# Kernel optimization log

Hardware: AMD Instinct MI355X
Metric: run time of the kernel (lower is better)

The kernel has to match this reference:

```python
import jax, jax.numpy as jnp
import numpy as np

N = 100000      # nodes
E = 1600000     # edges
D_IN = 256
D_HID = 256
D_OUT = 256
DROP_P = 0.5


def setup_inputs() -> dict:
    key = jax.random.key(0)
    ks = jax.random.split(key, 10)
    s = 1.0 / np.sqrt(D_HID)
    return {
        "z": jax.random.normal(ks[0], (N, D_OUT), jnp.float32),
        "omega": jax.random.normal(ks[1], (N, D_IN), jnp.float32),
        "edge_index": jax.random.randint(ks[2], (2, E), 0, N, jnp.int32),
        "W_lin": jax.random.normal(ks[3], (D_IN, D_HID), jnp.float32) * s,
        "b_lin": jnp.zeros((D_HID,), jnp.float32),
        "W_g1": jax.random.normal(ks[4], (D_HID, D_HID), jnp.float32) * s,
        "b_g1": jnp.zeros((D_HID,), jnp.float32),
        "W_g2": jax.random.normal(ks[5], (D_HID, D_OUT), jnp.float32) * s,
        "b_g2": jnp.zeros((D_OUT,), jnp.float32),
        "mask1": jax.random.bernoulli(ks[6], 1.0 - DROP_P, (N, D_HID)),
        "mask2": jax.random.bernoulli(ks[7], 1.0 - DROP_P, (N, D_HID)),
    }


def _gcn_norm(edge_index):
    # add self-loops, symmetric normalization deg^-1/2 * deg^-1/2
    loop = jnp.arange(N, dtype=edge_index.dtype)
    src = jnp.concatenate([edge_index[0], loop])
    dst = jnp.concatenate([edge_index[1], loop])
    deg = jax.ops.segment_sum(jnp.ones_like(dst, jnp.float32), dst, num_segments=N)
    dinv = jax.lax.rsqrt(deg)  # deg >= 1 because of self-loops
    norm = dinv[src] * dinv[dst]  # [E+N]
    return src, dst, norm


def _gcn_conv(x, W, b, src, dst, norm):
    h = x @ W                                  # [N, d_out]
    msg = h[src] * norm[:, None]               # gather over edges
    out = jax.ops.segment_sum(msg, dst, num_segments=N)  # scatter-add
    return out + b


def _dropout(x, mask):
    return jnp.where(mask, x * (1.0 / (1.0 - DROP_P)), 0.0)


def reference(z, omega, edge_index, W_lin, b_lin, W_g1, b_g1, W_g2, b_g2, mask1, mask2):
    src, dst, norm = _gcn_norm(edge_index)
    # layer 0: Linear + relu + dropout
    h = _dropout(jax.nn.relu(omega @ W_lin + b_lin), mask1)
    # layer 1: GCNConv + relu + dropout
    h = _dropout(jax.nn.relu(_gcn_conv(h, W_g1, b_g1, src, dst, norm)), mask2)
    # layer 2: GCNConv
    h = _gcn_conv(h, W_g2, b_g2, src, dst, norm)
    return z * h
```

## Files before the change

kernel.cpp:

```cpp
#include <hip/hip_runtime.h>
#include <stdint.h>

#define NN 100000
#define EE 1600000
#define DD 256
#define GB0 1563
#define NFILL 1024
#define NSUB 128

typedef __bf16 bf16;
typedef __attribute__((ext_vector_type(8))) __bf16 bf16x8;
typedef __attribute__((ext_vector_type(4))) float f32x4;
typedef __attribute__((ext_vector_type(4))) unsigned int u32x4;
typedef __attribute__((ext_vector_type(8))) unsigned short u16x8;

typedef __attribute__((address_space(1))) const unsigned int g_u32c;
typedef __attribute__((address_space(3))) unsigned int lds_u32;

__device__ __forceinline__ float bflo(unsigned int u) {
    union { unsigned int u; float f; } x; x.u = u << 16; return x.f;
}
__device__ __forceinline__ float bfhi(unsigned int u) {
    union { unsigned int u; float f; } x; x.u = u & 0xFFFF0000u; return x.f;
}
__device__ __forceinline__ unsigned short f2bf(float f) {
    return __builtin_bit_cast(unsigned short, (__bf16)f);
}

__global__ __launch_bounds__(256) void fillprep_k(
    const int* __restrict__ src, const int* __restrict__ dst,
    int* __restrict__ cnt, int* __restrict__ cs,
    const float* __restrict__ W0, const float* __restrict__ W1,
    const float* __restrict__ W2, bf16* __restrict__ T0,
    bf16* __restrict__ T1, bf16* __restrict__ T2,
    const unsigned int* __restrict__ m, int* __restrict__ flag) {
    int b = blockIdx.x;
    if (b < NFILL) {
        int prt = b & 7;
        int sub = b >> 3;
        int lo = prt * (NN >> 3);
        int hi = (prt == 7) ? NN : lo + (NN >> 3);
        const int per = EE / NSUB;
        int e0 = sub * per;
        int e1 = (sub == NSUB - 1) ? EE : e0 + per;
        for (int e = e0 + threadIdx.x; e < e1; e += 256) {
            int d = dst[e];
            if (d >= lo && d < hi) {
                int s = src[e];
                int slot = atomicAdd(&cnt[d], 1);
                if (slot < 64) cs[(d << 6) + slot] = s;
            }
        }
        return;
    }
    b -= NFILL;
    if (b == 192) {
        if (threadIdx.x < 64) {
            unsigned int v = m[threadIdx.x];
            int bad = (v > 1u && v != 0x3F800000u) ? 1 : 0;
            unsigned long long bl = __ballot(bad);
            if (threadIdx.x == 0) *flag = (bl != 0ull) ? 1 : 0;
        }
        return;
    }
    const float* W = b < 64 ? W0 : (b < 128 ? W1 : W2);
    bf16*       T  = b < 64 ? T0 : (b < 128 ? T1 : T2);
    int bb = b & 63;
    __shared__ float tile[32][33];
    int bx = bb & 7, by = bb >> 3;
    int tx = threadIdx.x & 31, ty = threadIdx.x >> 5;
    #pragma unroll
    for (int r = 0; r < 32; r += 8)
        tile[ty + r][tx] = W[(size_t)(by * 32 + ty + r) * DD + bx * 32 + tx];
    __syncthreads();
    #pragma unroll
    for (int r = 0; r < 32; r += 8)
        T[(size_t)(bx * 32 + ty + r) * DD + by * 32 + tx] = (bf16)tile[tx][ty + r];
}

template <int EPI, int F32A>
__device__ __forceinline__ void gemm_body(
    const void* __restrict__ Ap, const bf16* __restrict__ Wt,
    const float* __restrict__ bias, const void* __restrict__ mask,
    const int* __restrict__ flagp, const float* __restrict__ z,
    void* __restrict__ outp, bf16* As, bf16* Bs, int m0) {
    int tid = threadIdx.x;
    int wid = tid >> 6, lane = tid & 63;
    int lr = lane & 15, lk = lane >> 4;
    int rx = lr & 7;

    f32x4 acc[4][4] = {};

    for (int k0 = 0; k0 < DD; k0 += 64) {
        #pragma unroll
        for (int i = 0; i < 2; i++) {
            int f = i * 256 + tid;
            int row = f >> 3;
            int cl  = f & 7;
            int cg  = cl ^ (row & 7);
            int gr = m0 + row; if (gr > NN - 1) gr = NN - 1;
            if (F32A) {
                const float* sp = (const float*)Ap + (size_t)gr * DD + k0 + cl * 8;
                float4 v0 = *(const float4*)sp;
                float4 v1 = *(const float4*)(sp + 4);
                u16x8 o = { f2bf(v0.x), f2bf(v0.y), f2bf(v0.z), f2bf(v0.w),
                            f2bf(v1.x), f2bf(v1.y), f2bf(v1.z), f2bf(v1.w) };
                *(u16x8*)(As + row * 64 + cg * 8) = o;
            } else {
                __builtin_amdgcn_global_load_lds(
                    (g_u32c*)((const bf16*)Ap + (size_t)gr * DD + k0 + cg * 8),
                    (lds_u32*)(As + (size_t)f * 8), 16, 0, 0);
            }
        }
        #pragma unroll
        for (int i = 0; i < 8; i++) {
            int f = i * 256 + tid;
            int row = f >> 3;
            int cg  = (f & 7) ^ (row & 7);
            __builtin_amdgcn_global_load_lds(
                (g_u32c*)(Wt + (size_t)row * DD + k0 + cg * 8),
                (lds_u32*)(Bs + (size_t)f * 8), 16, 0, 0);
        }
        __syncthreads();
        #pragma unroll
        for (int kk = 0; kk < 2; kk++) {
            bf16x8 af[4], bfr[4];
            #pragma unroll
            for (int mi = 0; mi < 4; mi++)
                af[mi] = *(const bf16x8*)(As + (mi * 16 + lr) * 64 + (((kk * 4 + lk) ^ rx) * 8));
            #pragma unroll
            for (int ni = 0; ni < 4; ni++)
                bfr[ni] = *(const bf16x8*)(Bs + (wid * 64 + ni * 16 + lr) * 64 + (((kk * 4 + lk) ^ rx) * 8));
            #pragma unroll
            for (int mi = 0; mi < 4; mi++)
                #pragma unroll
                for (int ni = 0; ni < 4; ni++)
                    acc[mi][ni] = __builtin_amdgcn_mfma_f32_16x16x32_bf16(
                        bfr[ni], af[mi], acc[mi][ni], 0, 0, 0);
        }
        __syncthreads();
    }

    int bm = (EPI == 1) ? *flagp : 0;
    #pragma unroll
    for (int mi = 0; mi < 4; mi++) {
        int gr = m0 + mi * 16 + lr;
        if (gr >= NN) continue;
        #pragma unroll
        for (int ni = 0; ni < 4; ni++) {
            int gc = wid * 64 + ni * 16 + lk * 4;
            size_t idx = (size_t)gr * DD + gc;
            float4 b4 = *(const float4*)(bias + gc);
            float v0 = acc[mi][ni][0] + b4.x;
            float v1 = acc[mi][ni][1] + b4.y;
            float v2 = acc[mi][ni][2] + b4.z;
            float v3 = acc[mi][ni][3] + b4.w;
            if (EPI == 1) {
                v0 = fmaxf(v0, 0.f); v1 = fmaxf(v1, 0.f);
                v2 = fmaxf(v2, 0.f); v3 = fmaxf(v3, 0.f);
                if (bm) {
                    uchar4 u = *(const uchar4*)((const unsigned char*)mask + idx);
                    v0 *= u.x ? 2.f : 0.f; v1 *= u.y ? 2.f : 0.f;
                    v2 *= u.z ? 2.f : 0.f; v3 *= u.w ? 2.f : 0.f;
                } else {
                    uint4 u = *(const uint4*)((const unsigned int*)mask + idx);
                    v0 *= u.x ? 2.f : 0.f; v1 *= u.y ? 2.f : 0.f;
                    v2 *= u.z ? 2.f : 0.f; v3 *= u.w ? 2.f : 0.f;
                }
                ushort4 o = { f2bf(v0), f2bf(v1), f2bf(v2), f2bf(v3) };
                *(ushort4*)((unsigned short*)outp + idx) = o;
            } else {
                f32x4 zz = __builtin_nontemporal_load((const f32x4*)(z + idx));
                f32x4 o = { v0 * zz.x, v1 * zz.y, v2 * zz.z, v3 * zz.w };
                __builtin_nontemporal_store(o, (f32x4*)((float*)outp + idx));
            }
        }
    }
}

__global__ __launch_bounds__(256) void gemm0_k(
    const float* __restrict__ omega, const bf16* __restrict__ Wt,
    const float* __restrict__ bias, const void* __restrict__ mask,
    const int* __restrict__ flagp, bf16* __restrict__ outp) {
    __shared__ __align__(16) bf16 As[64 * 64];
    __shared__ __align__(16) bf16 Bs[256 * 64];
    int m0 = blockIdx.x * 64;
    if (m0 >= NN) return;
    gemm_body<1, 1>(omega, Wt, bias, mask, flagp, nullptr, outp, As, Bs, m0);
}

template <int ID, int EPI>
__global__ __launch_bounds__(256) void gemm_k(
    const bf16* __restrict__ Ap, const bf16* __restrict__ Wt,
    const float* __restrict__ bias, const void* __restrict__ mask,
    const int* __restrict__ flagp, const float* __restrict__ z,
    void* __restrict__ outp) {
    __shared__ __align__(16) bf16 As[64 * 64];
    __shared__ __align__(16) bf16 Bs[256 * 64];
    int m0 = blockIdx.x * 64;
    if (m0 >= NN) return;
    gemm_body<EPI, 0>(Ap, Wt, bias, mask, flagp, z, outp, As, Bs, m0);
}

#define AGG_GET(J, UVAR, MVAR)                                                   \
    {                                                                            \
        int _i = 2 * (J) + half;                                                 \
        int _s = __shfl(sl, _i & 63);                                            \
        float _w = __shfl(wl, _i & 63);                                          \
        MVAR = (_i < nume) ? _w : 0.f;                                           \
        UVAR = *(const u32x4*)(tb + (((size_t)(unsigned)_s) << 9) + lcoff);      \
    }
#define AGG_FMA(UVAR, MVAR)                                                      \
    {                                                                            \
        acc[0] = fmaf(MVAR, bflo(UVAR.x), acc[0]);                               \
        acc[1] = fmaf(MVAR, bfhi(UVAR.x), acc[1]);                               \
        acc[2] = fmaf(MVAR, bflo(UVAR.y), acc[2]);                               \
        acc[3] = fmaf(MVAR, bfhi(UVAR.y), acc[3]);                               \
        acc[4] = fmaf(MVAR, bflo(UVAR.z), acc[4]);                               \
        acc[5] = fmaf(MVAR, bfhi(UVAR.z), acc[5]);                               \
        acc[6] = fmaf(MVAR, bflo(UVAR.w), acc[6]);                               \
        acc[7] = fmaf(MVAR, bfhi(UVAR.w), acc[7]);                               \
    }

__global__ __launch_bounds__(256) void agg_k(
    const bf16* __restrict__ t, const int* __restrict__ cnt,
    const int* __restrict__ cs, bf16* __restrict__ out) {
    int node = blockIdx.x * 4 + (threadIdx.x >> 6);
    if (node >= NN) return;
    int lane = threadIdx.x & 63;
    int half = lane >> 5;
    int lc = lane & 31;
    int cn = cnt[node];
    int nume = cn > 63 ? 63 : cn;

    float acc[8] = {};
    const char* tb = (const char*)t;
    size_t lcoff = (size_t)(lc << 4);

    if (nume > 0) {
        int base = node << 6;
        int sl = 0; float wl = 0.f;
        if (lane < nume) {
            sl = __builtin_nontemporal_load(cs + base + lane);
            wl = rsqrtf((float)(cnt[sl] + 1));
        }
        int nit = (nume + 1) >> 1;

        u32x4 ua, ub, uc, ud;
        float ma, mb, mc, md;
        AGG_GET(0, ua, ma);
        AGG_GET(1, ub, mb);
        AGG_GET(2, uc, mc);
        int j = 0;
        for (; j + 3 < nit; j += 4) {
            AGG_GET(j + 3, ud, md); AGG_FMA(ua, ma);
            AGG_GET(j + 4, ua, ma); AGG_FMA(ub, mb);
            AGG_GET(j + 5, ub, mb); AGG_FMA(uc, mc);
            AGG_GET(j + 6, uc, mc); AGG_FMA(ud, md);
        }
        int rem = nit - j;
        if (rem > 0) AGG_FMA(ua, ma);
        if (rem > 1) AGG_FMA(ub, mb);
        if (rem > 2) AGG_FMA(uc, mc);
    }

    float dn = rsqrtf((float)(cn + 1));
    #pragma unroll
    for (int i = 0; i < 8; i++) acc[i] += __shfl_xor(acc[i], 32);
    if (half == 0) {
        u32x4 u = *(const u32x4*)(tb + (((size_t)(unsigned)node) << 9) + lcoff);
        acc[0] = fmaf(dn, bflo(u.x), acc[0]);
        acc[1] = fmaf(dn, bfhi(u.x), acc[1]);
        acc[2] = fmaf(dn, bflo(u.y), acc[2]);
        acc[3] = fmaf(dn, bfhi(u.y), acc[3]);
        acc[4] = fmaf(dn, bflo(u.z), acc[4]);
        acc[5] = fmaf(dn, bfhi(u.z), acc[5]);
        acc[6] = fmaf(dn, bflo(u.w), acc[6]);
        acc[7] = fmaf(dn, bfhi(u.w), acc[7]);
        #pragma unroll
        for (int i = 0; i < 8; i++) acc[i] *= dn;
        u16x8 o = { f2bf(acc[0]), f2bf(acc[1]), f2bf(acc[2]), f2bf(acc[3]),
                    f2bf(acc[4]), f2bf(acc[5]), f2bf(acc[6]), f2bf(acc[7]) };
        __builtin_nontemporal_store(o, (u16x8*)((unsigned short*)out + (size_t)node * DD + lc * 8));
    }
}

extern "C" void kernel_launch(void* const* d_in, const int* in_sizes, int n_in,
                              void* d_out, int out_size, void* d_ws, size_t ws_size,
                              hipStream_t stream) {
    const float* z     = (const float*)d_in[0];
    const float* omega = (const float*)d_in[1];
    const int*   eidx  = (const int*)d_in[2];
    const float* W_lin = (const float*)d_in[3];
    const float* b_lin = (const float*)d_in[4];
    const float* W_g1  = (const float*)d_in[5];
    const float* b_g1  = (const float*)d_in[6];
    const float* W_g2  = (const float*)d_in[7];
    const float* b_g2  = (const float*)d_in[8];
    const void*  mask1 = d_in[9];
    const void*  mask2 = d_in[10];

    const int* e_src = eidx;
    const int* e_dst = eidx + EE;

    char* p = (char*)d_ws;
    size_t off = 0;
    auto alloc = [&](size_t bytes) -> char* {
        char* r = p + off;
        off = (off + bytes + 255) & ~(size_t)255;
        return r;
    };
    int*   flag = (int*)  alloc(4);
    int*   cnt  = (int*)  alloc((size_t)NN * 4);
    int*   cs   = (int*)  alloc((size_t)NN * 64 * 4);
    bf16*  WtL  = (bf16*) alloc((size_t)DD * DD * 2);
    bf16*  Wt1  = (bf16*) alloc((size_t)DD * DD * 2);
    bf16*  Wt2  = (bf16*) alloc((size_t)DD * DD * 2);
    const size_t NBH = (size_t)NN * DD * 2;
    bf16*  S1   = (bf16*) alloc(NBH);
    bf16*  S2   = (bf16*) alloc(NBH);

    (void)hipMemsetAsync(cnt, 0, (size_t)NN * 4, stream);
    fillprep_k<<<NFILL + 193, 256, 0, stream>>>(e_src, e_dst, cnt, cs,
                                                W_lin, W_g1, W_g2, WtL, Wt1, Wt2,
                                                (const unsigned int*)mask1, flag);

    gemm0_k<<<GB0, 256, 0, stream>>>(omega, WtL, b_lin, mask1, flag, S1);
    agg_k<<<NN / 4, 256, 0, stream>>>(S1, cnt, cs, S2);
    gemm_k<1, 1><<<GB0, 256, 0, stream>>>(S2, Wt1, b_g1, mask2, flag, nullptr, S1);
    agg_k<<<NN / 4, 256, 0, stream>>>(S1, cnt, cs, S2);
    gemm_k<2, 2><<<GB0, 256, 0, stream>>>(S2, Wt2, b_g2, nullptr, flag, z, d_out);
}
```

Measured before the change: 552.8 us.

## Double-buffer GEMM LDS tiles with K=32 steps to overlap loads and MFMA

The GEMM main loop now uses two LDS buffers, each holding a K-slice of 32 instead of 64, so total LDS per block stays the same. The next slice is staged while MFMAs run on the current one. Swizzling is adapted to 4 chunks per row. The goal is to hide global-to-LDS load latency behind compute, at the cost of twice as many barriers per K and smaller per-step work.

```diff
diff --git a/kernel.cpp b/kernel.cpp
--- a/kernel.cpp
+++ b/kernel.cpp
@@ -83,61 +83,65 @@
     const void* __restrict__ Ap, const bf16* __restrict__ Wt,
     const float* __restrict__ bias, const void* __restrict__ mask,
     const int* __restrict__ flagp, const float* __restrict__ z,
-    void* __restrict__ outp, bf16* As, bf16* Bs, int m0) {
+    void* __restrict__ outp, bf16* AsBase, bf16* BsBase, int m0) {
     int tid = threadIdx.x;
     int wid = tid >> 6, lane = tid & 63;
     int lr = lane & 15, lk = lane >> 4;
-    int rx = lr & 7;
-
-    f32x4 acc[4][4] = {};
-
-    for (int k0 = 0; k0 < DD; k0 += 64) {
-        #pragma unroll
-        for (int i = 0; i < 2; i++) {
+
+    int arow = tid >> 2, ac = tid & 3;
+    int acg  = ac ^ (arow & 3);
+    int agr = m0 + arow; if (agr > NN - 1) agr = NN - 1;
+
+    auto stage = [&](int buf, int k0) {
+        bf16* As = AsBase + buf * (64 * 32);
+        bf16* Bs = BsBase + buf * (256 * 32);
+        if (F32A) {
+            const float* sp = (const float*)Ap + (size_t)agr * DD + k0 + ac * 8;
+            float4 v0 = *(const float4*)sp;
+            float4 v1 = *(const float4*)(sp + 4);
+            u16x8 o = { f2bf(v0.x), f2bf(v0.y), f2bf(v0.z), f2bf(v0.w),
+                        f2bf(v1.x), f2bf(v1.y), f2bf(v1.z), f2bf(v1.w) };
+            *(u16x8*)(As + arow * 32 + acg * 8) = o;
+        } else {
+            __builtin_amdgcn_global_load_lds(
+                (g_u32c*)((const bf16*)Ap + (size_t)agr * DD + k0 + acg * 8),
+                (lds_u32*)(As + (size_t)tid * 8), 16, 0, 0);
+        }
+        #pragma unroll
+        for (int i = 0; i < 4; i++) {
             int f = i * 256 + tid;
-            int row = f >> 3;
-            int cl  = f & 7;
-            int cg  = cl ^ (row & 7);
-            int gr = m0 + row; if (gr > NN - 1) gr = NN - 1;
-            if (F32A) {
-                const float* sp = (const float*)Ap + (size_t)gr * DD + k0 + cl * 8;
-                float4 v0 = *(const float4*)sp;
-                float4 v1 = *(const float4*)(sp + 4);
-                u16x8 o = { f2bf(v0.x), f2bf(v0.y), f2bf(v0.z), f2bf(v0.w),
-                            f2bf(v1.x), f2bf(v1.y), f2bf(v1.z), f2bf(v1.w) };
-                *(u16x8*)(As + row * 64 + cg * 8) = o;
-            } else {
-                __builtin_amdgcn_global_load_lds(
-                    (g_u32c*)((const bf16*)Ap + (size_t)gr * DD + k0 + cg * 8),
-                    (lds_u32*)(As + (size_t)f * 8), 16, 0, 0);
-            }
-        }
-        #pragma unroll
-        for (int i = 0; i < 8; i++) {
-            int f = i * 256 + tid;
-            int row = f >> 3;
-            int cg  = (f & 7) ^ (row & 7);
+            int row = f >> 2;
+            int cg  = (f & 3) ^ (row & 3);
             __builtin_amdgcn_global_load_lds(
                 (g_u32c*)(Wt + (size_t)row * DD + k0 + cg * 8),
                 (lds_u32*)(Bs + (size_t)f * 8), 16, 0, 0);
         }
-        __syncthreads();
-        #pragma unroll
-        for (int kk = 0; kk < 2; kk++) {
-            bf16x8 af[4], bfr[4];
-            #pragma unroll
-            for (int mi = 0; mi < 4; mi++)
-                af[mi] = *(const bf16x8*)(As + (mi * 16 + lr) * 64 + (((kk * 4 + lk) ^ rx) * 8));
+    };
+
+    f32x4 acc[4][4] = {};
+
+    stage(0, 0);
+    __syncthreads();
+    #pragma unroll
+    for (int step = 0; step < 8; step++) {
+        int cur = step & 1;
+        if (step < 7) stage(cur ^ 1, (step + 1) * 32);
+        const bf16* As = AsBase + cur * (64 * 32);
+        const bf16* Bs = BsBase + cur * (256 * 32);
+        bf16x8 af[4], bfr[4];
+        int rc = (lk ^ (lr & 3)) * 8;
+        #pragma unroll
+        for (int mi = 0; mi < 4; mi++)
+            af[mi] = *(const bf16x8*)(As + (mi * 16 + lr) * 32 + rc);
+        #pragma unroll
+        for (int ni = 0; ni < 4; ni++)
+            bfr[ni] = *(const bf16x8*)(Bs + (wid * 64 + ni * 16 + lr) * 32 + rc);
+        #pragma unroll
+        for (int mi = 0; mi < 4; mi++)
             #pragma unroll
             for (int ni = 0; ni < 4; ni++)
-                bfr[ni] = *(const bf16x8*)(Bs + (wid * 64 + ni * 16 + lr) * 64 + (((kk * 4 + lk) ^ rx) * 8));
-            #pragma unroll
-            for (int mi = 0; mi < 4; mi++)
-                #pragma unroll
-                for (int ni = 0; ni < 4; ni++)
-                    acc[mi][ni] = __builtin_amdgcn_mfma_f32_16x16x32_bf16(
-                        bfr[ni], af[mi], acc[mi][ni], 0, 0, 0);
-        }
+                acc[mi][ni] = __builtin_amdgcn_mfma_f32_16x16x32_bf16(
+                    bfr[ni], af[mi], acc[mi][ni], 0, 0, 0);
         __syncthreads();
     }
 
@@ -182,8 +186,8 @@
     const float* __restrict__ omega, const bf16* __restrict__ Wt,
     const float* __restrict__ bias, const void* __restrict__ mask,
     const int* __restrict__ flagp, bf16* __restrict__ outp) {
-    __shared__ __align__(16) bf16 As[64 * 64];
-    __shared__ __align__(16) bf16 Bs[256 * 64];
+    __shared__ __align__(16) bf16 As[2 * 64 * 32];
+    __shared__ __align__(16) bf16 Bs[2 * 256 * 32];
     int m0 = blockIdx.x * 64;
     if (m0 >= NN) return;
     gemm_body<1, 1>(omega, Wt, bias, mask, flagp, nullptr, outp, As, Bs, m0);
@@ -195,8 +199,8 @@
     const float* __restrict__ bias, const void* __restrict__ mask,
     const int* __restrict__ flagp, const float* __restrict__ z,
     void* __restrict__ outp) {
-    __shared__ __align__(16) bf16 As[64 * 64];
-    __shared__ __align__(16) bf16 Bs[256 * 64];
+    __shared__ __align__(16) bf16 As[2 * 64 * 32];
+    __shared__ __align__(16) bf16 Bs[2 * 256 * 32];
     int m0 = blockIdx.x * 64;
     if (m0 >= NN) return;
     gemm_body<EPI, 0>(Ap, Wt, bias, mask, flagp, z, outp, As, Bs, m0);
```

After: 565.2 us. 2.2% more time.
